# Optimization experiments

Measured on AMD Instinct MI355X. Metric: run time of the kernel, lower is better.

The kernel has to match this reference:

```python
import jax, jax.numpy as jnp
import numpy as np
from functools import partial

ALPHA = 0.5
BETA = 0.5
THRESHOLD = 0.5


def _ccl(fg):
    """Connected-component labeling (4-connectivity) of a 2D bool mask via
    iterative min-label propagation; background = 0, components get distinct
    positive ids (component-wise min of raster index + 1). Matches the
    component partition of scipy.ndimage.label (ids differ, masks identical)."""
    H, W = fg.shape
    BIG = H * W + 2
    init = jnp.where(fg, jnp.arange(1, H * W + 1, dtype=jnp.int32).reshape(H, W), 0)

    def step(lab):
        l = jnp.where(fg, lab, BIG)
        up = jnp.pad(l, ((1, 0), (0, 0)), constant_values=BIG)[:-1]
        dn = jnp.pad(l, ((0, 1), (0, 0)), constant_values=BIG)[1:]
        lf = jnp.pad(l, ((0, 0), (1, 0)), constant_values=BIG)[:, :-1]
        rt = jnp.pad(l, ((0, 0), (0, 1)), constant_values=BIG)[:, 1:]
        m = jnp.minimum(jnp.minimum(jnp.minimum(up, dn), jnp.minimum(lf, rt)), l)
        return jnp.where(fg, m, 0)

    def cond(c):
        return jnp.any(c[0] != c[1])

    def body(c):
        return (step(c[0]), c[0])

    lab, _ = jax.lax.while_loop(cond, body, (step(init), init))
    return lab


def _critical(a_lab, b_lab, n_seg):
    """Binary mask of components of a_lab that are not fully covered by the
    foreground of b_lab (i.e. contain at least one mistake voxel) -- the
    detect_critical split/merge criterion."""
    miss = ((b_lab == 0) & (a_lab > 0)).astype(jnp.int32)
    counts = jax.ops.segment_sum(miss.ravel(), a_lab.ravel(), num_segments=n_seg)
    return jnp.where(a_lab > 0, (counts[a_lab] > 0).astype(jnp.float32), 0.0)


def _critical_masks(preds, targets):
    # preds/targets: [B,1,H,W]; work on channel-0 2D slices as the module does
    p2 = preds[:, 0]
    t2 = targets[:, 0]
    H, W = p2.shape[-2:]
    n_seg = H * W + 1
    plab = jax.vmap(_ccl)(p2 > THRESHOLD)
    tlab = jax.vmap(_ccl)(t2 > 0)
    crit = jax.vmap(partial(_critical, n_seg=n_seg))
    neg = crit(tlab, plab)   # critical_type = -1: target components missed
    pos = crit(plab, tlab)   # critical_type = +1: pred components wrong
    return BETA * neg + (1.0 - BETA) * pos  # [B,H,W]


def setup_inputs() -> dict:
    key = jax.random.key(0)
    k1, k2 = jax.random.split(key)
    preds = jax.random.normal(k1, (16, 1, 1024, 1024), dtype=jnp.float32)
    targets = (jax.random.uniform(k2, (16, 1, 1024, 1024)) > 0.5).astype(jnp.float32)
    return {"preds": preds, "targets": targets}


def reference(preds, targets):
    # BCEWithLogitsLoss(reduction='none'), numerically stable
    loss = jnp.maximum(preds, 0) - preds * targets + jnp.log1p(jnp.exp(-jnp.abs(preds)))
    mask = _critical_masks(preds, targets)  # [B,H,W], constant wrt grads
    weight = (1.0 - ALPHA) + ALPHA * mask[:, None]  # broadcast over channel dim
    return (weight * loss).mean()
```

## Files before the change

### kernel.cpp

```cpp
#include <hip/hip_runtime.h>
#include <math.h>


#define HH 1024
#define WW 1024
#define IMGPIX (HH * WW)
#define NB_TOTAL 16
#define FLAGBIT 0x40000000
#define IDXMASK 0x3FFFFFFF
#define NBLK 2048
#define NPART 2048
#define NTHR 256
#define WPR 16
#define RPR 512
#define SROWS 32
#define STRIPS (HH / SROWS)
#define SLOTS (SROWS * RPR)
#define NTHR_S 1024

typedef unsigned long long u64;

__device__ __forceinline__ int findRootH(int* p, int i) {
    volatile int* vp = p;
    int r = i;
    int e = vp[r] & IDXMASK;
    while (e != r) {
        int e2 = vp[e] & IDXMASK;
        if (e2 != e) p[r] = e2;
        r = e; e = e2;
    }
    return r;
}

__device__ __forceinline__ void flagProp(int* p, int x) {
    while (true) {
        int r = findRootH(p, x);
        int old = atomicOr(&p[r], FLAGBIT);
        if ((old & IDXMASK) == r) return;
        x = old & IDXMASK;
    }
}

__device__ __forceinline__ void uniteGF(int* p, int a, int b) {
    int ra = findRootH(p, a), rb = findRootH(p, b);
    while (ra != rb) {
        if (ra < rb) { int t = ra; ra = rb; rb = t; }
        int e = p[ra];
        if ((e & IDXMASK) != ra) { ra = findRootH(p, e & IDXMASK); continue; }
        int prev = atomicCAS(&p[ra], e, rb);
        if (prev == e) {
            if (e & FLAGBIT) flagProp(p, rb);
            return;
        }
        ra = findRootH(p, prev & IDXMASK);
        rb = findRootH(p, rb);
    }
}

__device__ __forceinline__ int findRootL(int* lab, int i) {
    volatile int* vl = lab;
    int r = i;
    int e = vl[r] & IDXMASK;
    while (e != r) {
        int e2 = vl[e] & IDXMASK;
        if (e2 != e) lab[r] = e2;
        r = e; e = e2;
    }
    return r;
}

__device__ __forceinline__ void uniteL(int* lab, int a, int b) {
    int ra = findRootL(lab, a), rb = findRootL(lab, b);
    while (ra != rb) {
        if (ra < rb) { int t = ra; ra = rb; rb = t; }
        int prev = atomicCAS(&lab[ra], ra, rb);
        if (prev == ra) return;
        ra = findRootL(lab, prev & IDXMASK);
        rb = findRootL(lab, rb);
    }
}

__device__ __forceinline__ int runIndexW(u64 starts, int b) {
    u64 below = (2ULL << b) - 1ULL;
    return (int)__popcll(starts & below) - 1;
}

__global__ void k_zero(double* __restrict__ part) {
    part[blockIdx.x * blockDim.x + threadIdx.x] = 0.0;
}

__device__ __forceinline__ void phaseRuns(int lane, int mask, const float* lossv,
                                          long rbase, float* __restrict__ runsum,
                                          int* __restrict__ rcOut, int R,
                                          int& startsOut, int& exclOut) {
    int prevm = __shfl_up(mask, 1, 64);
    int carry = (lane == 0) ? 0 : ((prevm >> 15) & 1);
    int starts = mask & ~((mask << 1) | carry) & 0xFFFF;
    int cnt = __popc(starts);
    int incl = cnt;
    #pragma unroll
    for (int d = 1; d < 64; d <<= 1) {
        int u = __shfl_up(incl, d, 64);
        if (lane >= d) incl += u;
    }
    int excl = incl - cnt;
    float cur = 0.0f, headsum = 0.0f;
    bool begun = false, prevfg = (carry != 0), hasHead = false;
    int scount = 0;
    #pragma unroll
    for (int k = 0; k < 16; ++k) {
        bool fg = (mask >> k) & 1;
        if (fg) {
            if ((starts >> k) & 1) { cur = lossv[k]; begun = true; ++scount; }
            else cur += lossv[k];
        } else {
            if (prevfg) {
                if (begun) runsum[rbase + excl + scount - 1] = cur;
                else { hasHead = true; headsum = cur; }
            }
        }
        prevfg = fg;
    }
    float sv = prevfg ? cur : 0.0f;
    int fl = (starts != 0);
    #pragma unroll
    for (int d = 1; d < 64; d <<= 1) {
        float u = __shfl_up(sv, d, 64);
        int uf = __shfl_up(fl, d, 64);
        if (lane >= d) {
            if (!fl) sv += u;
            fl |= uf;
        }
    }
    float svprev = __shfl_up(sv, 1, 64);
    if (hasHead) runsum[rbase + excl - 1] = svprev + headsum;
    if (lane == 63) {
        if (prevfg) runsum[rbase + incl - 1] = sv;
        rcOut[R] = incl;
    }
    startsOut = starts;
    exclOut = excl;
}

__global__ void k_maskloss(const float* __restrict__ preds, const float* __restrict__ targets,
                           long gbase, int nrows,
                           u64* __restrict__ fT, u64* __restrict__ fP,
                           u64* __restrict__ sT, u64* __restrict__ sP,
                           int* __restrict__ prT, int* __restrict__ prP,
                           int* __restrict__ rcT, int* __restrict__ rcP,
                           float* __restrict__ runsumT, float* __restrict__ runsumP,
                           double* __restrict__ part) {
    __shared__ double sh[4];
    int wid = threadIdx.x >> 6, lane = threadIdx.x & 63;
    double lsum = 0.0;
    for (int R = blockIdx.x * 4 + wid; R < nrows; R += gridDim.x * 4) {
        long pixbase = (long)R * WW;
        long rbase = (long)R * RPR;
        const float4* p4 = (const float4*)(preds + gbase + pixbase);
        const float4* t4 = (const float4*)(targets + gbase + pixbase);
        float lossv[16];
        int maskT = 0, maskP = 0;
        float rowsum = 0.0f;
        #pragma unroll
        for (int j = 0; j < 4; ++j) {
            float4 pv = p4[lane * 4 + j];
            float4 tv = t4[lane * 4 + j];
            float pp[4] = {pv.x, pv.y, pv.z, pv.w};
            float tt[4] = {tv.x, tv.y, tv.z, tv.w};
            #pragma unroll
            for (int q = 0; q < 4; ++q) {
                int k = j * 4 + q;
                float p = pp[q], t = tt[q];
                float loss = fmaxf(p, 0.0f) - p * t + __logf(1.0f + __expf(-fabsf(p)));
                lossv[k] = loss;
                rowsum += loss;
                maskT |= ((int)(t > 0.0f)) << k;
                maskP |= ((int)(p > 0.5f)) << k;
            }
        }
        lsum += (double)rowsum;

        int stT_, exT, stP_, exP;
        phaseRuns(lane, maskT, lossv, rbase, runsumT, rcT, R, stT_, exT);
        phaseRuns(lane, maskP, lossv, rbase, runsumP, rcP, R, stP_, exP);

        int subid = lane & 15;
        int srcl = subid * 4;
        u64 fw = 0, sw = 0;
        #pragma unroll
        for (int j = 0; j < 4; ++j) {
            int mT = __shfl(maskT, srcl + j, 64);
            int mP = __shfl(maskP, srcl + j, 64);
            int aT = __shfl(stT_, srcl + j, 64);
            int aP = __shfl(stP_, srcl + j, 64);
            u64 m = (u64)(unsigned)((lane < 16) ? mT : mP);
            u64 a = (u64)(unsigned)((lane < 16) ? aT : aP);
            fw |= m << (16 * j);
            sw |= a << (16 * j);
        }
        int eT = __shfl(exT, srcl, 64);
        int eP = __shfl(exP, srcl, 64);
        int wi = R * WPR + subid;
        if (lane < 16) { fT[wi] = fw; sT[wi] = sw; prT[wi] = eT; }
        else if (lane < 32) { fP[wi] = fw; sP[wi] = sw; prP[wi] = eP; }
    }
    lsum *= 0.5;
    #pragma unroll
    for (int off = 32; off > 0; off >>= 1) lsum += __shfl_down(lsum, off, 64);
    if (lane == 0) sh[wid] = lsum;
    __syncthreads();
    if (threadIdx.x == 0) part[blockIdx.x] += sh[0] + sh[1] + sh[2] + sh[3];
}

__global__ __launch_bounds__(NTHR_S) void
k_strip(const u64* __restrict__ fT, const u64* __restrict__ fP,
        const u64* __restrict__ sT, const u64* __restrict__ sP,
        const int* __restrict__ prT, const int* __restrict__ prP,
        const int* __restrict__ rcT, const int* __restrict__ rcP,
        int* __restrict__ parentT, int* __restrict__ parentP) {
    __shared__ int lab[SLOTS];
    __shared__ int rcL[SROWS];
    int bid = blockIdx.x;
    int ph = bid & 1; bid >>= 1;
    int strip = bid & (STRIPS - 1);
    int img = bid >> 5;
    const u64* f = ph ? fP : fT;
    const u64* fB = ph ? fT : fP;
    const u64* s = ph ? sP : sT;
    const int* pr = ph ? prP : prT;
    const int* rc = ph ? rcP : rcT;
    int* parent = ph ? parentP : parentT;
    const int row0 = img * HH + strip * SROWS;

    if (threadIdx.x < SROWS) rcL[threadIdx.x] = rc[row0 + threadIdx.x];
    __syncthreads();

    for (int i = threadIdx.x; i < SLOTS; i += NTHR_S)
        if ((i & (RPR - 1)) < rcL[i >> 9]) lab[i] = i;
    __syncthreads();

    for (int task = threadIdx.x; task < (SROWS - 1) * WPR * 2; task += NTHR_S) {
        int j = task & 1, w = (task >> 1) & 15, r = task >> 5;
        int w0 = (row0 + r) * WPR + w, w1 = w0 + WPR;
        u64 o = f[w0] & f[w1];
        if (!o) continue;
        u64 s0 = s[w0], s1 = s[w1];
        int b0 = r * RPR + pr[w0], b1 = (r + 1) * RPR + pr[w1];
        u64 os = o & ~(o << 1);
        int k = 0;
        while (os) {
            int b = __builtin_ctzll(os);
            os &= os - 1;
            if ((k++ & 1) == j)
                uniteL(lab, b0 + runIndexW(s0, b), b1 + runIndexW(s1, b));
        }
    }
    __syncthreads();

    for (int task = threadIdx.x; task < SROWS * WPR * 2; task += NTHR_S) {
        int j = task & 1, w = (task >> 1) & 15, r = task >> 5;
        int wi = (row0 + r) * WPR + w;
        u64 m = f[wi] & ~fB[wi];
        if (!m) continue;
        u64 sw = s[wi];
        int base = r * RPR + pr[wi];
        u64 ms = m & ~(m << 1);
        int k = 0, last = -1;
        while (ms) {
            int b = __builtin_ctzll(ms);
            ms &= ms - 1;
            if ((k++ & 1) != j) continue;
            int rid = base + runIndexW(sw, b);
            if (rid == last) continue;
            last = rid;
            int rt = findRootL(lab, rid);
            if (!(((volatile int*)lab)[rt] & FLAGBIT)) atomicOr(&lab[rt], FLAGBIT);
        }
    }
    __syncthreads();

    const int gb = row0 * RPR;
    for (int i = threadIdx.x; i < SLOTS; i += NTHR_S) {
        if ((i & (RPR - 1)) >= rcL[i >> 9]) continue;
        int e = lab[i];
        int rt = e & IDXMASK;
        if (rt != i) rt = findRootL(lab, rt);
        parent[gb + i] = (rt == i) ? ((gb + i) | (e & FLAGBIT)) : (gb + rt);
    }
}

__global__ void k_bound(const u64* __restrict__ fT, const u64* __restrict__ fP,
                        const u64* __restrict__ sT, const u64* __restrict__ sP,
                        const int* __restrict__ prT, const int* __restrict__ prP,
                        int* __restrict__ parentT, int* __restrict__ parentP, int nb) {
    int tasks = nb * (STRIPS - 1) * WPR * 2;
    int stride = gridDim.x * blockDim.x;
    for (int id = blockIdx.x * blockDim.x + threadIdx.x; id < tasks; id += stride) {
        int ph = id & 1;
        int t = id >> 1;
        int w = t & 15; t >>= 4;
        int bnd = t % (STRIPS - 1);
        int img = t / (STRIPS - 1);
        int R = img * HH + bnd * SROWS + (SROWS - 1);
        const u64* f = ph ? fP : fT;
        const u64* s = ph ? sP : sT;
        const int* pr = ph ? prP : prT;
        int* parent = ph ? parentP : parentT;
        int w0 = R * WPR + w, w1 = w0 + WPR;
        u64 o = f[w0] & f[w1];
        if (!o) continue;
        u64 s0 = s[w0], s1 = s[w1];
        int b0 = R * RPR + pr[w0], b1 = (R + 1) * RPR + pr[w1];
        u64 os = o & ~(o << 1);
        while (os) {
            int b = __builtin_ctzll(os);
            os &= os - 1;
            uniteGF(parent, b0 + runIndexW(s0, b), b1 + runIndexW(s1, b));
        }
    }
}

__global__ void k_accumrun(const int* __restrict__ rcT, const int* __restrict__ rcP,
                           int* __restrict__ parentT, int* __restrict__ parentP,
                           const float* __restrict__ runsumT, const float* __restrict__ runsumP,
                           double* __restrict__ part, int nslots) {
    int stride = gridDim.x * blockDim.x;
    double local = 0.0;
    for (int i = blockIdx.x * blockDim.x + threadIdx.x; i < nslots; i += stride) {
        int row = i >> 9, k = i & (RPR - 1);
        if (k < rcT[row]) {
            int e = parentT[i];
            int r = e & IDXMASK;
            int fl;
            if (r == i) fl = e & FLAGBIT;
            else { r = findRootH(parentT, r); fl = parentT[r] & FLAGBIT; }
            if (fl) local += 0.25 * (double)runsumT[i];
        }
        if (k < rcP[row]) {
            int e = parentP[i];
            int r = e & IDXMASK;
            int fl;
            if (r == i) fl = e & FLAGBIT;
            else { r = findRootH(parentP, r); fl = parentP[r] & FLAGBIT; }
            if (fl) local += 0.25 * (double)runsumP[i];
        }
    }
    #pragma unroll
    for (int off = 32; off > 0; off >>= 1) local += __shfl_down(local, off, 64);
    __shared__ double sh[NTHR / 64];
    int lane = threadIdx.x & 63, wid = threadIdx.x >> 6;
    if (lane == 0) sh[wid] = local;
    __syncthreads();
    if (threadIdx.x == 0) {
        double tot = 0.0;
        #pragma unroll
        for (int w = 0; w < NTHR / 64; ++w) tot += sh[w];
        part[blockIdx.x] += tot;
    }
}

__global__ void k_final(const double* __restrict__ part, float* __restrict__ out, double inv_n) {
    double v = 0.0;
    for (int i = threadIdx.x; i < NPART; i += blockDim.x) v += part[i];
    #pragma unroll
    for (int off = 32; off > 0; off >>= 1) v += __shfl_down(v, off, 64);
    __shared__ double sh[NTHR / 64];
    int lane = threadIdx.x & 63, wid = threadIdx.x >> 6;
    if (lane == 0) sh[wid] = v;
    __syncthreads();
    if (threadIdx.x == 0) {
        double tot = 0.0;
        #pragma unroll
        for (int w = 0; w < NTHR / 64; ++w) tot += sh[w];
        out[0] = (float)(tot * inv_n);
    }
}

extern "C" void kernel_launch(void* const* d_in, const int* in_sizes, int n_in,
                              void* d_out, int out_size, void* d_ws, size_t ws_size,
                              hipStream_t stream) {
    const float* preds = (const float*)d_in[0];
    const float* targets = (const float*)d_in[1];
    float* out = (float*)d_out;

    double* part = (double*)d_ws;
    char* base = (char*)d_ws + NPART * sizeof(double);
    size_t avail = (ws_size > NPART * sizeof(double)) ? ws_size - NPART * sizeof(double) : 0;
    const size_t wpi = (size_t)HH * WPR;
    const size_t runs_pi = (size_t)HH * RPR;
    const size_t per_img = 4 * wpi * sizeof(u64) + 2 * wpi * sizeof(int)
                         + 2 * HH * sizeof(int) + 2 * runs_pi * sizeof(int)
                         + 2 * runs_pi * sizeof(float);
    int chunk = (int)(avail / per_img);
    if (chunk < 1) chunk = 1;
    if (chunk > NB_TOTAL) chunk = NB_TOTAL;

    u64* fT = (u64*)base;
    u64* fP = fT + (size_t)chunk * wpi;
    u64* sT = fP + (size_t)chunk * wpi;
    u64* sP = sT + (size_t)chunk * wpi;
    int* prT = (int*)(sP + (size_t)chunk * wpi);
    int* prP = prT + (size_t)chunk * wpi;
    int* rcT = prP + (size_t)chunk * wpi;
    int* rcP = rcT + (size_t)chunk * HH;
    int* parentT = rcP + (size_t)chunk * HH;
    int* parentP = parentT + (size_t)chunk * runs_pi;
    float* runsumT = (float*)(parentP + (size_t)chunk * runs_pi);
    float* runsumP = runsumT + (size_t)chunk * runs_pi;

    k_zero<<<NPART / NTHR, NTHR, 0, stream>>>(part);

    for (int b0 = 0; b0 < NB_TOTAL; b0 += chunk) {
        int nb = (b0 + chunk <= NB_TOTAL) ? chunk : (NB_TOTAL - b0);
        long gbase = (long)b0 * IMGPIX;
        int nrows = nb * HH;
        int nslots = (int)(nb * runs_pi);

        k_maskloss<<<NBLK, NTHR, 0, stream>>>(preds, targets, gbase, nrows,
                                              fT, fP, sT, sP, prT, prP, rcT, rcP,
                                              runsumT, runsumP, part);
        k_strip<<<nb * STRIPS * 2, NTHR_S, 0, stream>>>(fT, fP, sT, sP, prT, prP,
                                                        rcT, rcP, parentT, parentP);
        k_bound<<<128, NTHR, 0, stream>>>(fT, fP, sT, sP, prT, prP, parentT, parentP, nb);
        k_accumrun<<<NBLK, NTHR, 0, stream>>>(rcT, rcP, parentT, parentP,
                                              runsumT, runsumP, part, nslots);
    }

    double inv_n = 1.0 / ((double)NB_TOTAL * (double)IMGPIX);
    k_final<<<1, NTHR, 0, stream>>>(part, out, inv_n);
}
```

Before: 256.8 us.

## Pack per-run mistake flags into runsum sign bit and drop mistake-marking pass

Each run's loss sum now carries a 'contains mistake voxel' flag in its sign bit, computed during the mask/loss pass. The strip kernel then flags roots by reading runsum instead of making a separate bitmask scan over f & ~fB. The root-write step becomes two passes over the slots. k_accumrun reads parent and runsum as int4/float4 groups of four, and k_bound gets more blocks. The intent is to remove a strip-kernel phase with its sync, and to improve memory coalescing in the accumulation. The cost is extra sign-bit bookkeeping in the prefix scan and an extra loop with a barrier.

```diff
diff --git a/kernel.cpp b/kernel.cpp
--- a/kernel.cpp
+++ b/kernel.cpp
@@ -89,7 +89,12 @@
     part[blockIdx.x * blockDim.x + threadIdx.x] = 0.0;
 }
 
-__device__ __forceinline__ void phaseRuns(int lane, int mask, const float* lossv,
+__device__ __forceinline__ float packf(float mag, bool fl) {
+    return __uint_as_float(__float_as_uint(mag) | (fl ? 0x80000000u : 0u));
+}
+
+__device__ __forceinline__ void phaseRuns(int lane, int mask, int maskMist,
+                                          const float* lossv,
                                           long rbase, float* __restrict__ runsum,
                                           int* __restrict__ rcOut, int R,
                                           int& startsOut, int& exclOut) {
@@ -104,36 +109,46 @@
         if (lane >= d) incl += u;
     }
     int excl = incl - cnt;
-    float cur = 0.0f, headsum = 0.0f;
+    float cur = 0.0f, headmag = 0.0f;
+    bool curf = false, headf = false;
     bool begun = false, prevfg = (carry != 0), hasHead = false;
     int scount = 0;
     #pragma unroll
     for (int k = 0; k < 16; ++k) {
         bool fg = (mask >> k) & 1;
+        bool mk = (maskMist >> k) & 1;
         if (fg) {
-            if ((starts >> k) & 1) { cur = lossv[k]; begun = true; ++scount; }
-            else cur += lossv[k];
+            if ((starts >> k) & 1) { cur = lossv[k]; curf = mk; begun = true; ++scount; }
+            else { cur += lossv[k]; curf |= mk; }
         } else {
             if (prevfg) {
-                if (begun) runsum[rbase + excl + scount - 1] = cur;
-                else { hasHead = true; headsum = cur; }
+                if (begun) runsum[rbase + excl + scount - 1] = packf(cur, curf);
+                else { hasHead = true; headmag = cur; headf = curf; }
             }
         }
         prevfg = fg;
     }
-    float sv = prevfg ? cur : 0.0f;
+    float sv = prevfg ? packf(cur, curf) : 0.0f;
     int fl = (starts != 0);
     #pragma unroll
     for (int d = 1; d < 64; d <<= 1) {
         float u = __shfl_up(sv, d, 64);
         int uf = __shfl_up(fl, d, 64);
         if (lane >= d) {
-            if (!fl) sv += u;
+            if (!fl) {
+                unsigned sg = (__float_as_uint(sv) | __float_as_uint(u)) & 0x80000000u;
+                float mag = fabsf(sv) + fabsf(u);
+                sv = __uint_as_float(__float_as_uint(mag) | sg);
+            }
             fl |= uf;
         }
     }
     float svprev = __shfl_up(sv, 1, 64);
-    if (hasHead) runsum[rbase + excl - 1] = svprev + headsum;
+    if (hasHead) {
+        unsigned sg = (__float_as_uint(svprev) & 0x80000000u) | (headf ? 0x80000000u : 0u);
+        float mag = fabsf(svprev) + headmag;
+        runsum[rbase + excl - 1] = __uint_as_float(__float_as_uint(mag) | sg);
+    }
     if (lane == 63) {
         if (prevfg) runsum[rbase + incl - 1] = sv;
         rcOut[R] = incl;
@@ -180,9 +195,11 @@
         }
         lsum += (double)rowsum;
 
+        int mistT = maskT & ~maskP;
+        int mistP = maskP & ~maskT;
         int stT_, exT, stP_, exP;
-        phaseRuns(lane, maskT, lossv, rbase, runsumT, rcT, R, stT_, exT);
-        phaseRuns(lane, maskP, lossv, rbase, runsumP, rcP, R, stP_, exP);
+        phaseRuns(lane, maskT, mistT, lossv, rbase, runsumT, rcT, R, stT_, exT);
+        phaseRuns(lane, maskP, mistP, lossv, rbase, runsumP, rcP, R, stP_, exP);
 
         int subid = lane & 15;
         int srcl = subid * 4;
@@ -217,6 +234,7 @@
         const u64* __restrict__ sT, const u64* __restrict__ sP,
         const int* __restrict__ prT, const int* __restrict__ prP,
         const int* __restrict__ rcT, const int* __restrict__ rcP,
+        const float* __restrict__ runsumT, const float* __restrict__ runsumP,
         int* __restrict__ parentT, int* __restrict__ parentP) {
     __shared__ int lab[SLOTS];
     __shared__ int rcL[SROWS];
@@ -225,10 +243,10 @@
     int strip = bid & (STRIPS - 1);
     int img = bid >> 5;
     const u64* f = ph ? fP : fT;
-    const u64* fB = ph ? fT : fP;
     const u64* s = ph ? sP : sT;
     const int* pr = ph ? prP : prT;
     const int* rc = ph ? rcP : rcT;
+    const float* runsum = ph ? runsumP : runsumT;
     int* parent = ph ? parentP : parentT;
     const int row0 = img * HH + strip * SROWS;
 
@@ -257,35 +275,25 @@
     }
     __syncthreads();
 
-    for (int task = threadIdx.x; task < SROWS * WPR * 2; task += NTHR_S) {
-        int j = task & 1, w = (task >> 1) & 15, r = task >> 5;
-        int wi = (row0 + r) * WPR + w;
-        u64 m = f[wi] & ~fB[wi];
-        if (!m) continue;
-        u64 sw = s[wi];
-        int base = r * RPR + pr[wi];
-        u64 ms = m & ~(m << 1);
-        int k = 0, last = -1;
-        while (ms) {
-            int b = __builtin_ctzll(ms);
-            ms &= ms - 1;
-            if ((k++ & 1) != j) continue;
-            int rid = base + runIndexW(sw, b);
-            if (rid == last) continue;
-            last = rid;
-            int rt = findRootL(lab, rid);
-            if (!(((volatile int*)lab)[rt] & FLAGBIT)) atomicOr(&lab[rt], FLAGBIT);
-        }
-    }
-    __syncthreads();
-
     const int gb = row0 * RPR;
     for (int i = threadIdx.x; i < SLOTS; i += NTHR_S) {
         if ((i & (RPR - 1)) >= rcL[i >> 9]) continue;
         int e = lab[i];
         int rt = e & IDXMASK;
-        if (rt != i) rt = findRootL(lab, rt);
-        parent[gb + i] = (rt == i) ? ((gb + i) | (e & FLAGBIT)) : (gb + rt);
+        if (rt != i) {
+            rt = findRootL(lab, i);
+            parent[gb + i] = gb + rt;
+        }
+        if (__float_as_uint(runsum[gb + i]) >> 31) {
+            if (!(((volatile int*)lab)[rt] & FLAGBIT)) atomicOr(&lab[rt], FLAGBIT);
+        }
+    }
+    __syncthreads();
+
+    for (int i = threadIdx.x; i < SLOTS; i += NTHR_S) {
+        if ((i & (RPR - 1)) >= rcL[i >> 9]) continue;
+        int e = lab[i];
+        if ((e & IDXMASK) == i) parent[gb + i] = (gb + i) | (e & FLAGBIT);
     }
 }
 
@@ -326,23 +334,40 @@
                            double* __restrict__ part, int nslots) {
     int stride = gridDim.x * blockDim.x;
     double local = 0.0;
-    for (int i = blockIdx.x * blockDim.x + threadIdx.x; i < nslots; i += stride) {
-        int row = i >> 9, k = i & (RPR - 1);
-        if (k < rcT[row]) {
-            int e = parentT[i];
-            int r = e & IDXMASK;
-            int fl;
-            if (r == i) fl = e & FLAGBIT;
-            else { r = findRootH(parentT, r); fl = parentT[r] & FLAGBIT; }
-            if (fl) local += 0.25 * (double)runsumT[i];
-        }
-        if (k < rcP[row]) {
-            int e = parentP[i];
-            int r = e & IDXMASK;
-            int fl;
-            if (r == i) fl = e & FLAGBIT;
-            else { r = findRootH(parentP, r); fl = parentP[r] & FLAGBIT; }
-            if (fl) local += 0.25 * (double)runsumP[i];
+    int ngroups = nslots >> 2;
+    for (int g = blockIdx.x * blockDim.x + threadIdx.x; g < ngroups; g += stride) {
+        int base = g << 2;
+        int row = base >> 9, k = base & (RPR - 1);
+        int nT = rcT[row] - k, nP = rcP[row] - k;
+        if (nT > 0) {
+            int4 e4 = *(const int4*)&parentT[base];
+            float4 r4 = *(const float4*)&runsumT[base];
+            int ee[4] = {e4.x, e4.y, e4.z, e4.w};
+            float rr[4] = {r4.x, r4.y, r4.z, r4.w};
+            int n = nT < 4 ? nT : 4;
+            for (int j = 0; j < n; ++j) {
+                int e = ee[j];
+                int r = e & IDXMASK;
+                int fl;
+                if (r == base + j) fl = e & FLAGBIT;
+                else { r = findRootH(parentT, r); fl = parentT[r] & FLAGBIT; }
+                if (fl) local += 0.25 * (double)fabsf(rr[j]);
+            }
+        }
+        if (nP > 0) {
+            int4 e4 = *(const int4*)&parentP[base];
+            float4 r4 = *(const float4*)&runsumP[base];
+            int ee[4] = {e4.x, e4.y, e4.z, e4.w};
+            float rr[4] = {r4.x, r4.y, r4.z, r4.w};
+            int n = nP < 4 ? nP : 4;
+            for (int j = 0; j < n; ++j) {
+                int e = ee[j];
+                int r = e & IDXMASK;
+                int fl;
+                if (r == base + j) fl = e & FLAGBIT;
+                else { r = findRootH(parentP, r); fl = parentP[r] & FLAGBIT; }
+                if (fl) local += 0.25 * (double)fabsf(rr[j]);
+            }
         }
     }
     #pragma unroll
@@ -420,8 +445,9 @@
                                               fT, fP, sT, sP, prT, prP, rcT, rcP,
                                               runsumT, runsumP, part);
         k_strip<<<nb * STRIPS * 2, NTHR_S, 0, stream>>>(fT, fP, sT, sP, prT, prP,
-                                                        rcT, rcP, parentT, parentP);
-        k_bound<<<128, NTHR, 0, stream>>>(fT, fP, sT, sP, prT, prP, parentT, parentP, nb);
+                                                        rcT, rcP, runsumT, runsumP,
+                                                        parentT, parentP);
+        k_bound<<<512, NTHR, 0, stream>>>(fT, fP, sT, sP, prT, prP, parentT, parentP, nb);
         k_accumrun<<<NBLK, NTHR, 0, stream>>>(rcT, rcP, parentT, parentP,
                                               runsumT, runsumP, part, nslots);
     }
```

Result: faster. 243.8 us (-5.1%).
